# Optimization experiments

Measured on AMD Instinct MI355X. Metric: run time of the kernel, lower is better.

Reference implementation:

```python
import jax, jax.numpy as jnp
import numpy as np

SCORE_THRESHOLD = 0.5
IOU_THRESHOLD = 0.5


def _pairwise_iou(boxes):
    # boxes: [N, 4] in xyxy
    x1, y1, x2, y2 = boxes[:, 0], boxes[:, 1], boxes[:, 2], boxes[:, 3]
    area = (x2 - x1) * (y2 - y1)  # [N]
    ix1 = jnp.maximum(x1[:, None], x1[None, :])
    iy1 = jnp.maximum(y1[:, None], y1[None, :])
    ix2 = jnp.minimum(x2[:, None], x2[None, :])
    iy2 = jnp.minimum(y2[:, None], y2[None, :])
    iw = jnp.clip(ix2 - ix1, 0.0)
    ih = jnp.clip(iy2 - iy1, 0.0)
    inter = iw * ih  # [N, N]
    union = area[:, None] + area[None, :] - inter
    return inter / jnp.maximum(union, 1e-9)


def setup_inputs() -> dict:
    key = jax.random.key(0)
    rtdetr_raw_out = jax.random.uniform(key, (1, 8192, 5), dtype=jnp.float32)
    return {"rtdetr_raw_out": rtdetr_raw_out}


def reference(rtdetr_raw_out):
    x = rtdetr_raw_out[0]                      # [N, 5]
    cxcywh = x[:, :4]
    conf = x[:, 4]
    conf = conf / jnp.max(conf)                # normalize by max score
    cx, cy, w, h = cxcywh[:, 0], cxcywh[:, 1], cxcywh[:, 2], cxcywh[:, 3]
    xyxy = jnp.stack([cx - w * 0.5, cy - h * 0.5, cx + w * 0.5, cy + h * 0.5], axis=1)
    valid = conf >= SCORE_THRESHOLD            # score filter
    N = xyxy.shape[0]
    # sort by descending score (torchvision nms processes boxes in score order)
    order = jnp.argsort(-conf)
    boxes_s = xyxy[order]
    scores_s = conf[order]
    valid_s = valid[order]
    iou = _pairwise_iou(boxes_s)               # [N, N]
    idx = jnp.arange(N)

    def body(i, keep):
        # if box i survives, suppress all lower-score boxes with IoU > thr
        sup = keep[i] & (iou[i] > IOU_THRESHOLD) & (idx > i)
        return keep & ~sup

    keep = jax.lax.fori_loop(0, N, body, valid_s)
    out = jnp.concatenate([boxes_s, scores_s[:, None]], axis=1)  # [N, 5]
    # fixed-shape output: suppressed / below-threshold rows are zeroed
    return jnp.where(keep[:, None], out, 0.0)
```

## Files before the change

kernel.cpp:

```cpp
#include <hip/hip_runtime.h>
#include <cstdint>

typedef unsigned long long ull;

#define N_BOX 8192
#define N_WORDS 128
#define CH 512
#define WPC 8

#define OFF_TB     0
#define OFF_TD     3932160
#define OFF_BOXES  4456448
#define OFF_SCORES 4587520
#define OFF_RANK   4620288
#define OFF_MAXC   4653056

__device__ __forceinline__ int rows_before(int c) {
    return 8192 * c - 256 * c * (c + 1);
}

__device__ __forceinline__ ull make_key(float s, int idx) {
    return (((ull)__float_as_uint(s)) << 13) | (ull)(8191 - idx);
}

__device__ __forceinline__ float box_area(float4 b) {
    return __fmul_rn(__fsub_rn(b.z, b.x), __fsub_rn(b.w, b.y));
}

__device__ __forceinline__ bool iou_gt_half(float4 a, float aarea, float4 b, float barea) {
    float ix1 = fmaxf(a.x, b.x);
    float iy1 = fmaxf(a.y, b.y);
    float ix2 = fminf(a.z, b.z);
    float iy2 = fminf(a.w, b.w);
    float iw = fmaxf(__fsub_rn(ix2, ix1), 0.0f);
    float ih = fmaxf(__fsub_rn(iy2, iy1), 0.0f);
    float inter = __fmul_rn(iw, ih);
    float uni = __fsub_rn(__fadd_rn(aarea, barea), inter);
    float iou = __fdiv_rn(inter, fmaxf(uni, 1e-9f));
    return iou > 0.5f;
}

__global__ __launch_bounds__(1024) void k1_max_zero(const float* __restrict__ in,
                                                    float* __restrict__ maxc,
                                                    int* __restrict__ rank) {
    int t = threadIdx.x;
    float m = 0.0f;
    for (int k = t; k < N_BOX; k += 1024) m = fmaxf(m, in[k * 5 + 4]);
    for (int off = 32; off; off >>= 1) m = fmaxf(m, __shfl_down(m, off));
    __shared__ float wm[16];
    if ((t & 63) == 0) wm[t >> 6] = m;
    __syncthreads();
    if (t == 0) {
        float mm = wm[0];
        for (int k = 1; k < 16; ++k) mm = fmaxf(mm, wm[k]);
        *maxc = mm;
    }
    for (int k = t; k < N_BOX; k += 1024) rank[k] = 0;
}

__global__ __launch_bounds__(256) void k2_rank(const float* __restrict__ in,
                                               const float* __restrict__ maxc_p,
                                               int* __restrict__ rank) {
    __shared__ ull keys[1024];
    int t = threadIdx.x;
    int bx = blockIdx.x;
    int it = bx & 31;
    int jt = bx >> 5;
    float maxc = *maxc_p;
    for (int r = 0; r < 4; ++r) {
        int j = jt * 1024 + r * 256 + t;
        float s = __fdiv_rn(in[j * 5 + 4], maxc);
        keys[r * 256 + t] = make_key(s, j);
    }
    __syncthreads();
    int i = it * 256 + t;
    ull ki = make_key(__fdiv_rn(in[i * 5 + 4], maxc), i);
    int cnt = 0;
    #pragma unroll 8
    for (int k = 0; k < 1024; ++k) cnt += (keys[k] > ki) ? 1 : 0;
    atomicAdd(&rank[i], cnt);
}

__global__ __launch_bounds__(256) void k3_scatter(const float* __restrict__ in,
                                                  const int* __restrict__ rank,
                                                  const float* __restrict__ maxc_p,
                                                  float4* __restrict__ boxes4,
                                                  float* __restrict__ scores) {
    int i = blockIdx.x * 256 + threadIdx.x;
    float cx = in[i * 5 + 0];
    float cy = in[i * 5 + 1];
    float w  = in[i * 5 + 2];
    float h  = in[i * 5 + 3];
    float c  = in[i * 5 + 4];
    float maxc = *maxc_p;
    float s = __fdiv_rn(c, maxc);
    int r = rank[i];
    float4 b;
    b.x = __fsub_rn(cx, __fmul_rn(w, 0.5f));
    b.y = __fsub_rn(cy, __fmul_rn(h, 0.5f));
    b.z = __fadd_rn(cx, __fmul_rn(w, 0.5f));
    b.w = __fadd_rn(cy, __fmul_rn(h, 0.5f));
    boxes4[r] = b;
    scores[r] = s;
}

__global__ __launch_bounds__(256) void k4_build(const float4* __restrict__ boxes4,
                                                const float* __restrict__ scores,
                                                ull* __restrict__ TB,
                                                ull* __restrict__ TD) {
    __shared__ float4 sb[CH];
    __shared__ float sa[CH];
    int bid = blockIdx.x;
    int t = threadIdx.x;
    int c, j0;
    bool diag;
    if (bid >= 1920) {
        diag = true;
        int d = bid - 1920;
        c = d >> 4;
        j0 = (d & 15) * 32;
    } else {
        diag = false;
        c = 0;
        int rem = bid;
        while (rem >= 240 - 16 * c) { rem -= 240 - 16 * c; ++c; }
        j0 = CH * (c + 1) + rem * 32;
    }
    if (scores[c * CH] < 0.5f) return;
    if (!diag && scores[j0] < 0.5f) return;

    for (int i = t; i < CH; i += 256) {
        float4 b = boxes4[c * CH + i];
        sb[i] = b;
        sa[i] = box_area(b);
    }
    __syncthreads();

    int w = t & 7;
    int jj = j0 + (t >> 3);
    if (diag) {
        int jl = jj;
        float4 me = sb[jl];
        float ma = sa[jl];
        int wj = jl >> 6;
        int lim = (w < wj) ? 64 : ((w == wj) ? (jl & 63) : 0);
        ull bits = 0;
        for (int k = 0; k < lim; ++k)
            if (iou_gt_half(sb[w * 64 + k], sa[w * 64 + k], me, ma)) bits |= 1ull << k;
        TD[c * 4096 + w * 512 + jl] = bits;
    } else {
        int j = jj;
        float4 me = boxes4[j];
        float ma = box_area(me);
        ull bits = 0;
        for (int k = 0; k < 64; ++k)
            if (iou_gt_half(sb[w * 64 + k], sa[w * 64 + k], me, ma)) bits |= 1ull << k;
        TB[(size_t)(rows_before(c) + (j - CH * (c + 1))) * WPC + w] = bits;
    }
}

__global__ __launch_bounds__(1024) void k5_nms(const float4* __restrict__ boxes4,
                                               const float* __restrict__ scores,
                                               const ull* __restrict__ TBg,
                                               const ull* __restrict__ TDg,
                                               float* __restrict__ out) {
    __shared__ ull TDb[2][CH * WPC];
    __shared__ unsigned amask32[2 * N_WORDS];
    __shared__ ull keptA[WPC];
    __shared__ ull keptB[WPC];
    __shared__ int svb;
    int t = threadIdx.x;
    int lane = t & 63;
    int wave = t >> 6;

    if (t == 0) svb = 0;
    __syncthreads();
    {
        int cnt = 0;
        #pragma unroll
        for (int k = 0; k < 8; ++k) cnt += (scores[k * 1024 + t] >= 0.5f) ? 1 : 0;
        for (int off = 32; off; off >>= 1) cnt += __shfl_down(cnt, off);
        if (lane == 0) atomicAdd(&svb, cnt);
    }
    __syncthreads();
    int vb = svb;

    if (t < 2 * N_WORDS) {
        int n = vb - t * 32;
        amask32[t] = (n >= 32) ? 0xffffffffu : ((n <= 0) ? 0u : ((1u << n) - 1u));
    }
    if (t < WPC) { keptA[t] = 0; keptB[t] = 0; }
    for (int i2 = t; i2 < CH * WPC; i2 += 1024) TDb[0][i2] = TDg[i2];
    __syncthreads();

    int nchv = (vb + CH - 1) / CH;
    int cur = 0;
    for (int c = 0; c < nchv; ++c) {
        if (wave == 0) {
            const ull* T = TDb[cur];
            ull alive[WPC];
            #pragma unroll
            for (int w = 0; w < WPC; ++w)
                alive[w] = (ull)amask32[c * 16 + 2 * w] |
                           ((ull)amask32[c * 16 + 2 * w + 1] << 32);
            #pragma unroll
            for (int w = 0; w < WPC; ++w) {
                ull word = alive[w];
                if (!word) continue;
                ull Tc[WPC];
                #pragma unroll
                for (int j = 0; j < WPC; ++j)
                    if (j >= w) Tc[j] = T[w * 512 + j * 64 + lane];
                ull td = Tc[w];
                ull a2 = word, kept = 0;
                while (a2 & ~kept) {
                    bool al = (a2 >> lane) & 1;
                    bool kp = (kept >> lane) & 1;
                    ull nk = __ballot(al && !kp && ((td & a2) == 0));
                    ull nd = __ballot(al && !kp && ((td & kept) != 0));
                    kept |= nk;
                    a2 &= ~nd;
                }
                alive[w] = kept;
                #pragma unroll
                for (int j = 0; j < WPC; ++j) {
                    if (j <= w) continue;
                    if (!alive[j]) continue;
                    alive[j] &= ~__ballot((Tc[j] & kept) != 0);
                }
            }
            if (lane == 0) {
                #pragma unroll
                for (int w = 0; w < WPC; ++w) {
                    amask32[c * 16 + 2 * w]     = (unsigned)alive[w];
                    amask32[c * 16 + 2 * w + 1] = (unsigned)(alive[w] >> 32);
                    keptA[w] = alive[w];
                }
            }
        } else if (wave < 8) {
            if (c > 0) {
                ull kw[WPC];
                ull anyk = 0;
                #pragma unroll
                for (int k = 0; k < WPC; ++k) { kw[k] = keptB[k]; anyk |= kw[k]; }
                if (anyk) {
                    const ull* TBc = TBg + (size_t)rows_before(c - 1) * WPC;
                    int jbase = CH * c;
                    int jstart = CH * (c + 1);
                    for (int j = jstart + (t - 64); j < vb; j += 448) {
                        if ((amask32[j >> 5] >> (j & 31)) & 1u) {
                            const ull* r = TBc + (size_t)(j - jbase) * WPC;
                            ull acc = 0;
                            #pragma unroll
                            for (int k = 0; k < WPC; ++k) acc |= r[k] & kw[k];
                            if (acc) atomicAnd(&amask32[j >> 5], ~(1u << (j & 31)));
                        }
                    }
                }
            }
        } else {
            if (c + 1 < nchv) {
                int base = (c + 1) * CH * WPC;
                for (int i2 = t - 512; i2 < CH * WPC; i2 += 512)
                    TDb[cur ^ 1][i2] = TDg[base + i2];
            }
        }
        __syncthreads();

        if (c + 1 < nchv) {
            ull kw[WPC];
            ull anyk = 0;
            #pragma unroll
            for (int k = 0; k < WPC; ++k) { kw[k] = keptA[k]; anyk |= kw[k]; }
            if (anyk) {
                const ull* TBc = TBg + (size_t)rows_before(c) * WPC;
                int jbase = CH * (c + 1);
                int jend = jbase + CH;
                if (jend > vb) jend = vb;
                for (int j = jbase + t; j < jend; j += 1024) {
                    if ((amask32[j >> 5] >> (j & 31)) & 1u) {
                        const ull* r = TBc + (size_t)(j - jbase) * WPC;
                        ull acc = 0;
                        #pragma unroll
                        for (int k = 0; k < WPC; ++k) acc |= r[k] & kw[k];
                        if (acc) atomicAnd(&amask32[j >> 5], ~(1u << (j & 31)));
                    }
                }
            }
        }
        if (t < WPC) keptB[t] = keptA[t];
        cur ^= 1;
        __syncthreads();
    }

    #pragma unroll
    for (int rr = 0; rr < 8; ++rr) {
        int j = t * 8 + rr;
        bool kept = (amask32[j >> 5] >> (j & 31)) & 1u;
        float4 b = boxes4[j];
        float s = scores[j];
        out[j * 5 + 0] = kept ? b.x : 0.0f;
        out[j * 5 + 1] = kept ? b.y : 0.0f;
        out[j * 5 + 2] = kept ? b.z : 0.0f;
        out[j * 5 + 3] = kept ? b.w : 0.0f;
        out[j * 5 + 4] = kept ? s   : 0.0f;
    }
}

extern "C" void kernel_launch(void* const* d_in, const int* in_sizes, int n_in,
                              void* d_out, int out_size, void* d_ws, size_t ws_size,
                              hipStream_t stream) {
    const float* in = (const float*)d_in[0];
    char* ws = (char*)d_ws;
    ull* TB        = (ull*)(ws + OFF_TB);
    ull* TD        = (ull*)(ws + OFF_TD);
    float4* boxes4 = (float4*)(ws + OFF_BOXES);
    float* scores  = (float*)(ws + OFF_SCORES);
    int* rank      = (int*)(ws + OFF_RANK);
    float* maxc    = (float*)(ws + OFF_MAXC);
    float* out     = (float*)d_out;

    k1_max_zero<<<1, 1024, 0, stream>>>(in, maxc, rank);
    k2_rank<<<256, 256, 0, stream>>>(in, maxc, rank);
    k3_scatter<<<32, 256, 0, stream>>>(in, rank, maxc, boxes4, scores);
    k4_build<<<2176, 256, 0, stream>>>(boxes4, scores, TB, TD);
    k5_nms<<<1, 1024, 0, stream>>>(boxes4, scores, TB, TD, out);
}
```

Baseline: 137.2 us.

## Fuse max, rank sort and scatter into one kernel with per-block valid counts

Replaces the three pre-processing kernels (max reduction, rank counting, scatter) with a single 64-block kernel. Each block recomputes the global max, builds all 8192 sort keys in shared memory, ranks its 128 boxes with 8-way split counting, scatters them, and writes a per-block count of valid boxes. The NMS kernel then sums these 64 partial counts instead of rescanning all 8192 scores, and its prologue is reordered so there is one fewer barrier. This removes two launches and the global rank atomics, at the cost of every block redundantly reading all the scores and filling a 64 KB shared-memory key array.

```diff
diff --git a/kernel.cpp b/kernel.cpp
--- a/kernel.cpp
+++ b/kernel.cpp
@@ -12,8 +12,7 @@
 #define OFF_TD     3932160
 #define OFF_BOXES  4456448
 #define OFF_SCORES 4587520
-#define OFF_RANK   4620288
-#define OFF_MAXC   4653056
+#define OFF_VBPART 4620288
 
 __device__ __forceinline__ int rows_before(int c) {
     return 8192 * c - 256 * c * (c + 1);
@@ -40,68 +39,71 @@
     return iou > 0.5f;
 }
 
-__global__ __launch_bounds__(1024) void k1_max_zero(const float* __restrict__ in,
-                                                    float* __restrict__ maxc,
-                                                    int* __restrict__ rank) {
+__global__ __launch_bounds__(1024) void ka_sort(const float* __restrict__ in,
+                                                float4* __restrict__ boxes4,
+                                                float* __restrict__ scores,
+                                                int* __restrict__ vbpart) {
+    __shared__ ull skeys[N_BOX];
+    __shared__ float wm[16];
+    __shared__ int rnk[128];
+    __shared__ int vcnt;
     int t = threadIdx.x;
+    int bid = blockIdx.x;
+
+    float cf[8];
     float m = 0.0f;
-    for (int k = t; k < N_BOX; k += 1024) m = fmaxf(m, in[k * 5 + 4]);
+    #pragma unroll
+    for (int k = 0; k < 8; ++k) {
+        cf[k] = in[(k * 1024 + t) * 5 + 4];
+        m = fmaxf(m, cf[k]);
+    }
     for (int off = 32; off; off >>= 1) m = fmaxf(m, __shfl_down(m, off));
-    __shared__ float wm[16];
     if ((t & 63) == 0) wm[t >> 6] = m;
-    __syncthreads();
-    if (t == 0) {
-        float mm = wm[0];
-        for (int k = 1; k < 16; ++k) mm = fmaxf(mm, wm[k]);
-        *maxc = mm;
-    }
-    for (int k = t; k < N_BOX; k += 1024) rank[k] = 0;
-}
-
-__global__ __launch_bounds__(256) void k2_rank(const float* __restrict__ in,
-                                               const float* __restrict__ maxc_p,
-                                               int* __restrict__ rank) {
-    __shared__ ull keys[1024];
-    int t = threadIdx.x;
-    int bx = blockIdx.x;
-    int it = bx & 31;
-    int jt = bx >> 5;
-    float maxc = *maxc_p;
-    for (int r = 0; r < 4; ++r) {
-        int j = jt * 1024 + r * 256 + t;
-        float s = __fdiv_rn(in[j * 5 + 4], maxc);
-        keys[r * 256 + t] = make_key(s, j);
-    }
-    __syncthreads();
-    int i = it * 256 + t;
-    ull ki = make_key(__fdiv_rn(in[i * 5 + 4], maxc), i);
-    int cnt = 0;
-    #pragma unroll 8
-    for (int k = 0; k < 1024; ++k) cnt += (keys[k] > ki) ? 1 : 0;
-    atomicAdd(&rank[i], cnt);
-}
-
-__global__ __launch_bounds__(256) void k3_scatter(const float* __restrict__ in,
-                                                  const int* __restrict__ rank,
-                                                  const float* __restrict__ maxc_p,
-                                                  float4* __restrict__ boxes4,
-                                                  float* __restrict__ scores) {
-    int i = blockIdx.x * 256 + threadIdx.x;
-    float cx = in[i * 5 + 0];
-    float cy = in[i * 5 + 1];
-    float w  = in[i * 5 + 2];
-    float h  = in[i * 5 + 3];
-    float c  = in[i * 5 + 4];
-    float maxc = *maxc_p;
-    float s = __fdiv_rn(c, maxc);
-    int r = rank[i];
-    float4 b;
-    b.x = __fsub_rn(cx, __fmul_rn(w, 0.5f));
-    b.y = __fsub_rn(cy, __fmul_rn(h, 0.5f));
-    b.z = __fadd_rn(cx, __fmul_rn(w, 0.5f));
-    b.w = __fadd_rn(cy, __fmul_rn(h, 0.5f));
-    boxes4[r] = b;
-    scores[r] = s;
+    if (t < 128) rnk[t] = 0;
+    if (t == 0) vcnt = 0;
+    __syncthreads();
+    float maxc = wm[0];
+    #pragma unroll
+    for (int k = 1; k < 16; ++k) maxc = fmaxf(maxc, wm[k]);
+
+    #pragma unroll
+    for (int k = 0; k < 8; ++k) {
+        int j = k * 1024 + t;
+        skeys[j] = make_key(__fdiv_rn(cf[k], maxc), j);
+    }
+    __syncthreads();
+
+    {
+        int il = t & 127;
+        ull ki = skeys[bid * 128 + il];
+        int q = t >> 7;
+        int cnt = 0;
+        #pragma unroll 8
+        for (int k = q * 1024; k < (q + 1) * 1024; ++k)
+            cnt += (skeys[k] > ki) ? 1 : 0;
+        atomicAdd(&rnk[il], cnt);
+    }
+    __syncthreads();
+
+    if (t < 128) {
+        int i = bid * 128 + t;
+        float cx = in[i * 5 + 0];
+        float cy = in[i * 5 + 1];
+        float w  = in[i * 5 + 2];
+        float h  = in[i * 5 + 3];
+        float s  = __fdiv_rn(in[i * 5 + 4], maxc);
+        int r = rnk[t];
+        float4 b;
+        b.x = __fsub_rn(cx, __fmul_rn(w, 0.5f));
+        b.y = __fsub_rn(cy, __fmul_rn(h, 0.5f));
+        b.z = __fadd_rn(cx, __fmul_rn(w, 0.5f));
+        b.w = __fadd_rn(cy, __fmul_rn(h, 0.5f));
+        boxes4[r] = b;
+        scores[r] = s;
+        if (s >= 0.5f) atomicAdd(&vcnt, 1);
+    }
+    __syncthreads();
+    if (t == 0) vbpart[bid] = vcnt;
 }
 
 __global__ __launch_bounds__(256) void k4_build(const float4* __restrict__ boxes4,
@@ -163,6 +165,7 @@
                                                const float* __restrict__ scores,
                                                const ull* __restrict__ TBg,
                                                const ull* __restrict__ TDg,
+                                               const int* __restrict__ vbpart,
                                                float* __restrict__ out) {
     __shared__ ull TDb[2][CH * WPC];
     __shared__ unsigned amask32[2 * N_WORDS];
@@ -173,15 +176,13 @@
     int lane = t & 63;
     int wave = t >> 6;
 
-    if (t == 0) svb = 0;
-    __syncthreads();
-    {
-        int cnt = 0;
-        #pragma unroll
-        for (int k = 0; k < 8; ++k) cnt += (scores[k * 1024 + t] >= 0.5f) ? 1 : 0;
-        for (int off = 32; off; off >>= 1) cnt += __shfl_down(cnt, off);
-        if (lane == 0) atomicAdd(&svb, cnt);
-    }
+    if (t < 64) {
+        int v = vbpart[t];
+        for (int off = 32; off; off >>= 1) v += __shfl_down(v, off);
+        if (t == 0) svb = v;
+    }
+    for (int i2 = t; i2 < CH * WPC; i2 += 1024) TDb[0][i2] = TDg[i2];
+    if (t < WPC) { keptA[t] = 0; keptB[t] = 0; }
     __syncthreads();
     int vb = svb;
 
@@ -189,8 +190,6 @@
         int n = vb - t * 32;
         amask32[t] = (n >= 32) ? 0xffffffffu : ((n <= 0) ? 0u : ((1u << n) - 1u));
     }
-    if (t < WPC) { keptA[t] = 0; keptB[t] = 0; }
-    for (int i2 = t; i2 < CH * WPC; i2 += 1024) TDb[0][i2] = TDg[i2];
     __syncthreads();
 
     int nchv = (vb + CH - 1) / CH;
@@ -316,13 +315,10 @@
     ull* TD        = (ull*)(ws + OFF_TD);
     float4* boxes4 = (float4*)(ws + OFF_BOXES);
     float* scores  = (float*)(ws + OFF_SCORES);
-    int* rank      = (int*)(ws + OFF_RANK);
-    float* maxc    = (float*)(ws + OFF_MAXC);
+    int* vbpart    = (int*)(ws + OFF_VBPART);
     float* out     = (float*)d_out;
 
-    k1_max_zero<<<1, 1024, 0, stream>>>(in, maxc, rank);
-    k2_rank<<<256, 256, 0, stream>>>(in, maxc, rank);
-    k3_scatter<<<32, 256, 0, stream>>>(in, rank, maxc, boxes4, scores);
+    ka_sort<<<64, 1024, 0, stream>>>(in, boxes4, scores, vbpart);
     k4_build<<<2176, 256, 0, stream>>>(boxes4, scores, TB, TD);
-    k5_nms<<<1, 1024, 0, stream>>>(boxes4, scores, TB, TD, out);
-}
+    k5_nms<<<1, 1024, 0, stream>>>(boxes4, scores, TB, TD, vbpart, out);
+}
```

Result: no change. 139.8 us (+1.9%).

## Split adjacent-chunk suppression into transposed TC tiles handled by the serial wave

Applied to the files above, without the earlier changes.

Pulls the next-chunk cross-suppression masks out of the row-major TB into a separate transposed TC layout, prefetched into shared memory together with TD. Wave 0 now applies the previous chunk's kept bits to the current chunk using ballots over the TC tiles. This removes the second per-chunk phase and one __syncthreads from the sequential NMS loop. The cost is serial ballot work in wave 0 and twice the shared-memory staging. The k4 build kernel is re-partitioned so TB covers only chunk pairs at distance two or more.

```diff
diff --git a/kernel.cpp b/kernel.cpp
--- a/kernel.cpp
+++ b/kernel.cpp
@@ -9,14 +9,15 @@
 #define WPC 8
 
 #define OFF_TB     0
+#define OFF_TC     3440640
 #define OFF_TD     3932160
 #define OFF_BOXES  4456448
 #define OFF_SCORES 4587520
 #define OFF_RANK   4620288
 #define OFF_MAXC   4653056
 
-__device__ __forceinline__ int rows_before(int c) {
-    return 8192 * c - 256 * c * (c + 1);
+__device__ __forceinline__ int rows_before2(int c) {
+    return 7424 * c - 256 * c * c;
 }
 
 __device__ __forceinline__ ull make_key(float s, int idx) {
@@ -107,27 +108,34 @@
 __global__ __launch_bounds__(256) void k4_build(const float4* __restrict__ boxes4,
                                                 const float* __restrict__ scores,
                                                 ull* __restrict__ TB,
+                                                ull* __restrict__ TC,
                                                 ull* __restrict__ TD) {
     __shared__ float4 sb[CH];
     __shared__ float sa[CH];
     int bid = blockIdx.x;
     int t = threadIdx.x;
-    int c, j0;
-    bool diag;
+    int c;
+    int mode;
+    int j0;
     if (bid >= 1920) {
-        diag = true;
+        mode = 2;
         int d = bid - 1920;
         c = d >> 4;
         j0 = (d & 15) * 32;
+    } else if (bid >= 1680) {
+        mode = 1;
+        int d = bid - 1680;
+        c = d >> 4;
+        j0 = (d & 15) * 32;
     } else {
-        diag = false;
+        mode = 0;
         c = 0;
         int rem = bid;
-        while (rem >= 240 - 16 * c) { rem -= 240 - 16 * c; ++c; }
-        j0 = CH * (c + 1) + rem * 32;
+        while (rem >= 224 - 16 * c) { rem -= 224 - 16 * c; ++c; }
+        j0 = CH * (c + 2) + rem * 32;
     }
     if (scores[c * CH] < 0.5f) return;
-    if (!diag && scores[j0] < 0.5f) return;
+    if (mode == 0 && scores[j0] < 0.5f) return;
 
     for (int i = t; i < CH; i += 256) {
         float4 b = boxes4[c * CH + i];
@@ -137,9 +145,9 @@
     __syncthreads();
 
     int w = t & 7;
-    int jj = j0 + (t >> 3);
-    if (diag) {
-        int jl = jj;
+    int r = t >> 3;
+    if (mode == 2) {
+        int jl = j0 + r;
         float4 me = sb[jl];
         float ma = sa[jl];
         int wj = jl >> 6;
@@ -148,26 +156,36 @@
         for (int k = 0; k < lim; ++k)
             if (iou_gt_half(sb[w * 64 + k], sa[w * 64 + k], me, ma)) bits |= 1ull << k;
         TD[c * 4096 + w * 512 + jl] = bits;
-    } else {
-        int j = jj;
+    } else if (mode == 1) {
+        int jl = j0 + r;
+        int j = CH * (c + 1) + jl;
         float4 me = boxes4[j];
         float ma = box_area(me);
         ull bits = 0;
         for (int k = 0; k < 64; ++k)
             if (iou_gt_half(sb[w * 64 + k], sa[w * 64 + k], me, ma)) bits |= 1ull << k;
-        TB[(size_t)(rows_before(c) + (j - CH * (c + 1))) * WPC + w] = bits;
+        TC[c * 4096 + w * 512 + jl] = bits;
+    } else {
+        int j = j0 + r;
+        float4 me = boxes4[j];
+        float ma = box_area(me);
+        ull bits = 0;
+        for (int k = 0; k < 64; ++k)
+            if (iou_gt_half(sb[w * 64 + k], sa[w * 64 + k], me, ma)) bits |= 1ull << k;
+        TB[(size_t)(rows_before2(c) + (j - CH * (c + 2))) * WPC + w] = bits;
     }
 }
 
 __global__ __launch_bounds__(1024) void k5_nms(const float4* __restrict__ boxes4,
                                                const float* __restrict__ scores,
                                                const ull* __restrict__ TBg,
+                                               const ull* __restrict__ TCg,
                                                const ull* __restrict__ TDg,
                                                float* __restrict__ out) {
     __shared__ ull TDb[2][CH * WPC];
+    __shared__ ull TCb[2][CH * WPC];
     __shared__ unsigned amask32[2 * N_WORDS];
-    __shared__ ull keptA[WPC];
-    __shared__ ull keptB[WPC];
+    __shared__ ull keptbuf[2][WPC];
     __shared__ int svb;
     int t = threadIdx.x;
     int lane = t & 63;
@@ -182,6 +200,8 @@
         for (int off = 32; off; off >>= 1) cnt += __shfl_down(cnt, off);
         if (lane == 0) atomicAdd(&svb, cnt);
     }
+    for (int i2 = t; i2 < CH * WPC; i2 += 1024) TDb[0][i2] = TDg[i2];
+    if (t < WPC) { keptbuf[0][t] = 0; keptbuf[1][t] = 0; }
     __syncthreads();
     int vb = svb;
 
@@ -189,20 +209,32 @@
         int n = vb - t * 32;
         amask32[t] = (n >= 32) ? 0xffffffffu : ((n <= 0) ? 0u : ((1u << n) - 1u));
     }
-    if (t < WPC) { keptA[t] = 0; keptB[t] = 0; }
-    for (int i2 = t; i2 < CH * WPC; i2 += 1024) TDb[0][i2] = TDg[i2];
     __syncthreads();
 
     int nchv = (vb + CH - 1) / CH;
-    int cur = 0;
     for (int c = 0; c < nchv; ++c) {
+        int cur = c & 1;
         if (wave == 0) {
-            const ull* T = TDb[cur];
             ull alive[WPC];
             #pragma unroll
             for (int w = 0; w < WPC; ++w)
                 alive[w] = (ull)amask32[c * 16 + 2 * w] |
                            ((ull)amask32[c * 16 + 2 * w + 1] << 32);
+            if (c > 0) {
+                const ull* kb = keptbuf[(c - 1) & 1];
+                const ull* TCc = TCb[cur];
+                #pragma unroll
+                for (int w = 0; w < WPC; ++w) {
+                    ull kw = kb[w];
+                    if (!kw) continue;
+                    #pragma unroll
+                    for (int v = 0; v < WPC; ++v) {
+                        ull m = TCc[w * 512 + v * 64 + lane];
+                        alive[v] &= ~__ballot((m & kw) != 0);
+                    }
+                }
+            }
+            const ull* T = TDb[cur];
             #pragma unroll
             for (int w = 0; w < WPC; ++w) {
                 ull word = alive[w];
@@ -234,20 +266,20 @@
                 for (int w = 0; w < WPC; ++w) {
                     amask32[c * 16 + 2 * w]     = (unsigned)alive[w];
                     amask32[c * 16 + 2 * w + 1] = (unsigned)(alive[w] >> 32);
-                    keptA[w] = alive[w];
+                    keptbuf[c & 1][w] = alive[w];
                 }
             }
         } else if (wave < 8) {
-            if (c > 0) {
+            if (c > 0 && c - 1 <= 13) {
+                const ull* kb = keptbuf[(c - 1) & 1];
                 ull kw[WPC];
                 ull anyk = 0;
                 #pragma unroll
-                for (int k = 0; k < WPC; ++k) { kw[k] = keptB[k]; anyk |= kw[k]; }
+                for (int k = 0; k < WPC; ++k) { kw[k] = kb[k]; anyk |= kw[k]; }
                 if (anyk) {
-                    const ull* TBc = TBg + (size_t)rows_before(c - 1) * WPC;
-                    int jbase = CH * c;
-                    int jstart = CH * (c + 1);
-                    for (int j = jstart + (t - 64); j < vb; j += 448) {
+                    const ull* TBc = TBg + (size_t)rows_before2(c - 1) * WPC;
+                    int jbase = CH * (c + 1);
+                    for (int j = jbase + (t - 64); j < vb; j += 448) {
                         if ((amask32[j >> 5] >> (j & 31)) & 1u) {
                             const ull* r = TBc + (size_t)(j - jbase) * WPC;
                             ull acc = 0;
@@ -260,36 +292,16 @@
             }
         } else {
             if (c + 1 < nchv) {
-                int base = (c + 1) * CH * WPC;
-                for (int i2 = t - 512; i2 < CH * WPC; i2 += 512)
-                    TDb[cur ^ 1][i2] = TDg[base + i2];
+                const ull* tdsrc = TDg + (c + 1) * CH * WPC;
+                const ull* tcsrc = TCg + c * CH * WPC;
+                ull* tddst = TDb[cur ^ 1];
+                ull* tcdst = TCb[cur ^ 1];
+                for (int i2 = t - 512; i2 < CH * WPC; i2 += 512) {
+                    tddst[i2] = tdsrc[i2];
+                    tcdst[i2] = tcsrc[i2];
+                }
             }
         }
-        __syncthreads();
-
-        if (c + 1 < nchv) {
-            ull kw[WPC];
-            ull anyk = 0;
-            #pragma unroll
-            for (int k = 0; k < WPC; ++k) { kw[k] = keptA[k]; anyk |= kw[k]; }
-            if (anyk) {
-                const ull* TBc = TBg + (size_t)rows_before(c) * WPC;
-                int jbase = CH * (c + 1);
-                int jend = jbase + CH;
-                if (jend > vb) jend = vb;
-                for (int j = jbase + t; j < jend; j += 1024) {
-                    if ((amask32[j >> 5] >> (j & 31)) & 1u) {
-                        const ull* r = TBc + (size_t)(j - jbase) * WPC;
-                        ull acc = 0;
-                        #pragma unroll
-                        for (int k = 0; k < WPC; ++k) acc |= r[k] & kw[k];
-                        if (acc) atomicAnd(&amask32[j >> 5], ~(1u << (j & 31)));
-                    }
-                }
-            }
-        }
-        if (t < WPC) keptB[t] = keptA[t];
-        cur ^= 1;
         __syncthreads();
     }
 
@@ -313,6 +325,7 @@
     const float* in = (const float*)d_in[0];
     char* ws = (char*)d_ws;
     ull* TB        = (ull*)(ws + OFF_TB);
+    ull* TC        = (ull*)(ws + OFF_TC);
     ull* TD        = (ull*)(ws + OFF_TD);
     float4* boxes4 = (float4*)(ws + OFF_BOXES);
     float* scores  = (float*)(ws + OFF_SCORES);
@@ -323,6 +336,6 @@
     k1_max_zero<<<1, 1024, 0, stream>>>(in, maxc, rank);
     k2_rank<<<256, 256, 0, stream>>>(in, maxc, rank);
     k3_scatter<<<32, 256, 0, stream>>>(in, rank, maxc, boxes4, scores);
-    k4_build<<<2176, 256, 0, stream>>>(boxes4, scores, TB, TD);
-    k5_nms<<<1, 1024, 0, stream>>>(boxes4, scores, TB, TD, out);
-}
+    k4_build<<<2176, 256, 0, stream>>>(boxes4, scores, TB, TC, TD);
+    k5_nms<<<1, 1024, 0, stream>>>(boxes4, scores, TB, TC, TD, out);
+}
```

Result: no change. 136.2 us (-0.7%).
